# Optimization experiments

Measured on AMD Instinct MI355X. Metric: run time of the kernel, lower is better.

## Reference

```python
import jax, jax.numpy as jnp
import numpy as np

DIM = 2048
HEAD_DIM = 128
H = DIM // HEAD_DIM          # num ttt heads = 16
D_H = 128                    # inter_multi = 1.0 -> d_h = head_dim
CHUNK = 2048                 # lact_chunk_size
B, L = 1, 8192
BASE_LR = 0.01
LN_EPS = 1e-6                # flax LayerNorm default
NS_COEFS = [(4.0848, -6.8946, 2.927), (3.9505, -6.3029, 2.6377),
            (3.7418, -5.5913, 2.3037), (2.8769, -3.1427, 1.2046),
            (2.8366, -3.0525, 1.2012)]


def silu(x):
    return x * jax.nn.sigmoid(x)


def silu_backprop(dy, x):
    s = jax.nn.sigmoid(x)
    return dy * s * (1 + x * (1 - s))


def l2_norm(x, eps=1e-5):
    return x / (jnp.linalg.norm(x, axis=-1, keepdims=True) + eps)


def zeropower_ns5(G):
    # 5-step Newton-Schulz orthogonalization on a batch of matrices (bh, m, n)
    X = G
    transposed = G.shape[1] > G.shape[2]
    if transposed:
        X = jnp.swapaxes(X, 1, 2)
    X = X / (jnp.linalg.norm(X, axis=(1, 2), keepdims=True) + 1e-7)
    for a, b, c in NS_COEFS:
        A = X @ jnp.swapaxes(X, 1, 2)
        Bm = b * A + c * (A @ A)
        X = a * X + Bm @ X
    if transposed:
        X = jnp.swapaxes(X, 1, 2)
    return X


def block_causal_lact_swiglu(w0, w1, w2, q, k, v, lr0, lr1, lr2, momentum):
    # w0,w2: (bh, d_h, d); w1: (bh, d, d_h); q,k,v: (bh, l, d); lr*: (bh, l, 1)
    bh, l, d = k.shape
    v = jnp.swapaxes(v, 1, 2)   # (bh, d, l)
    q = jnp.swapaxes(q, 1, 2)   # (bh, d, l)
    w0_norm = jnp.linalg.norm(w0, axis=2, keepdims=True)
    w1_norm = jnp.linalg.norm(w1, axis=2, keepdims=True)
    w2_norm = jnp.linalg.norm(w2, axis=2, keepdims=True)
    outs = []
    for i in range(0, l - CHUNK, CHUNK):
        s, e = i, i + CHUNK
        ki = k[:, s:e, :]                      # (bh, C, d)
        vi = v[:, :, s:e]                      # (bh, d, C)
        qi = q[:, :, s:e]                      # (bh, d, C)
        lr0i, lr1i, lr2i = lr0[:, s:e, :], lr1[:, s:e, :], lr2[:, s:e, :]
        # apply current fast weights to queries
        h = w2 @ qi                            # (bh, d_h, C)
        gate = silu(w0 @ qi)
        outs.append(w1 @ (gate * h))           # (bh, d, C)
        # manual SwiGLU backprop through keys to get fast-weight grads
        kiT = jnp.swapaxes(ki, 1, 2)           # (bh, d, C)
        gate_before = w0 @ kiT                 # (bh, d_h, C)
        hidden_before = w2 @ kiT               # (bh, d_h, C)
        hidden = silu(gate_before) * hidden_before
        dhidden = jnp.swapaxes(w1, 1, 2) @ vi  # (bh, d_h, C)
        dhidden_before = dhidden * silu(gate_before)
        dgate = dhidden * hidden_before
        dgate_before = silu_backprop(dgate, gate_before)
        lr1iT = jnp.swapaxes(lr1i, 1, 2)       # (bh, 1, C) per-token lr
        dw1 = vi @ jnp.swapaxes(hidden * lr1iT, 1, 2)   # (bh, d, d_h)
        dw0 = dgate_before @ (ki * lr0i)                # (bh, d_h, d)
        dw2 = dhidden_before @ (ki * lr2i)              # (bh, d_h, d)
        if momentum is not None:
            m_i = jnp.mean(momentum[:, s:e, :], axis=1, keepdims=True)  # (bh,1,1)
            dw0 = dw0 + dw0 * m_i
            dw1 = dw1 + dw1 * m_i
            dw2 = dw2 + dw2 * m_i
        dw0 = zeropower_ns5(dw0)
        dw1 = zeropower_ns5(dw1)
        dw2 = zeropower_ns5(dw2)
        w0 = w0 + dw0
        w1 = w1 + dw1
        w2 = w2 + dw2
        # renormalize rows back to the initial norms
        w0 = w0 / (jnp.linalg.norm(w0, axis=2, keepdims=True) + 1e-5) * w0_norm
        w1 = w1 / (jnp.linalg.norm(w1, axis=2, keepdims=True) + 1e-5) * w1_norm
        w2 = w2 / (jnp.linalg.norm(w2, axis=2, keepdims=True) + 1e-5) * w2_norm
    # final chunk: apply only
    qi = q[:, :, l - CHUNK:]
    h = w2 @ qi
    gate = silu(w0 @ qi)
    outs.append(w1 @ (gate * h))
    out = jnp.concatenate(outs, axis=2)        # (bh, d, l)
    return jnp.swapaxes(out, 1, 2)             # (bh, l, d)


def _forward(x, W_qkv, W_lr, W_o, W_m, b_m, W_s, b_s, ln_g, ln_b, w0, w1, w2):
    b, l, _ = x.shape
    h, d = H, HEAD_DIM
    qkv = silu(x @ W_qkv).reshape(b, l, h, 3 * d)
    ttt_q, ttt_k, ttt_v = jnp.split(qkv, 3, axis=-1)
    ttt_q = l2_norm(ttt_q).reshape(b * h, l, d)
    ttt_k = l2_norm(ttt_k).reshape(b * h, l, d)
    ttt_v = ttt_v.reshape(b * h, l, d)
    base_lr_inv = BASE_LR + jnp.log(-jnp.expm1(jnp.float32(-BASE_LR)))
    lr = jax.nn.softplus(x @ W_lr + base_lr_inv)                 # (b, l, 3h)
    lr = lr.reshape(b, l, 3, h).transpose(2, 0, 3, 1).reshape(3, b * h, l, 1)
    lr0, lr1, lr2 = lr[0], lr[1], lr[2]
    w0b = jnp.tile(w0, (b, 1, 1))
    w1b = jnp.tile(w1, (b, 1, 1))
    w2b = jnp.tile(w2, (b, 1, 1))
    momentum = jax.nn.sigmoid(x @ W_m + b_m)                     # (b, l, h)
    momentum = momentum.reshape(b, l, h, 1).transpose(0, 2, 1, 3).reshape(b * h, l, 1)
    out = block_causal_lact_swiglu(w0b, w1b, w2b, ttt_q, ttt_k, ttt_v,
                                   lr0, lr1, lr2, momentum)      # (bh, l, d)
    # LayerNorm over last dim (flax default eps)
    mu = jnp.mean(out, axis=-1, keepdims=True)
    var = jnp.mean(jnp.square(out - mu), axis=-1, keepdims=True)
    out = (out - mu) * jax.lax.rsqrt(var + LN_EPS) * ln_g + ln_b
    scale = silu(x @ W_s + b_s).reshape(b, l, h, 1).transpose(0, 2, 1, 3).reshape(b * h, l, 1)
    out = out * scale
    out = out.reshape(b, h, l, d).transpose(0, 2, 1, 3).reshape(b, l, h * d)
    return out @ W_o


def setup_inputs() -> dict:
    ks = jax.random.split(jax.random.key(0), 11)
    sd = 1.0 / np.sqrt(DIM)
    return {
        "x": jax.random.normal(ks[0], (B, L, DIM), jnp.float32),
        "W_qkv": jax.random.normal(ks[1], (DIM, 3 * DIM), jnp.float32) * sd,
        "W_lr": jax.random.normal(ks[2], (DIM, 3 * H), jnp.float32) * sd,
        "W_o": jax.random.normal(ks[3], (DIM, DIM), jnp.float32) * sd,
        "W_m": jax.random.normal(ks[4], (DIM, H), jnp.float32) * sd,
        "b_m": jnp.zeros((H,), jnp.float32),
        "W_s": jax.random.normal(ks[5], (DIM, H), jnp.float32) * sd,
        "b_s": jnp.zeros((H,), jnp.float32),
        "ln_g": jnp.ones((HEAD_DIM,), jnp.float32),
        "ln_b": jnp.zeros((HEAD_DIM,), jnp.float32),
        "w0": jax.random.normal(ks[6], (H, D_H, HEAD_DIM), jnp.float32) / np.sqrt(HEAD_DIM),
        "w1": jax.random.normal(ks[7], (H, HEAD_DIM, D_H), jnp.float32) / np.sqrt(D_H),
        "w2": jax.random.normal(ks[8], (H, D_H, HEAD_DIM), jnp.float32) / np.sqrt(HEAD_DIM),
    }


def reference(x, W_qkv, W_lr, W_o, W_m, b_m, W_s, b_s, ln_g, ln_b, w0, w1, w2):
    return _forward(x, W_qkv, W_lr, W_o, W_m, b_m, W_s, b_s, ln_g, ln_b, w0, w1, w2)
```

## Files before the change

### kernel.cpp

```cpp
#include <hip/hip_runtime.h>
#include <hip/hip_bf16.h>
#include <cstdint>
#include <cstddef>

#define LSEQ   8192
#define DMODEL 2048
#define NH     16
#define HD     128
#define CH     2048

typedef __attribute__((ext_vector_type(8))) __bf16 bf16x8;
typedef __attribute__((ext_vector_type(4))) float f32x4;


__device__ __forceinline__ float wave_sum64(float v) {
#pragma unroll
  for (int m = 32; m; m >>= 1) v += __shfl_xor(v, m, 64);
  return v;
}

__device__ __forceinline__ float sigm(float x) { return 1.0f / (1.0f + expf(-x)); }

__device__ __forceinline__ unsigned short f2bf(float f) {
  unsigned int u = __float_as_uint(f);
  u += 0x7FFFu + ((u >> 16) & 1u);
  return (unsigned short)(u >> 16);
}
__device__ __forceinline__ float bf2f(unsigned short h) {
  return __uint_as_float((unsigned int)h << 16);
}

__device__ __forceinline__ void gload_lds16(const void* g, void* l) {
  __builtin_amdgcn_global_load_lds((__attribute__((address_space(1))) void*)(g),
                                   (__attribute__((address_space(3))) void*)(l), 16, 0, 0);
}

union bfu8 { bf16x8 v; unsigned short u[8]; };


__global__ void k_cast(const float* __restrict__ X, unsigned short* __restrict__ Xb, int n4) {
  int i = blockIdx.x * 256 + threadIdx.x;
  int stride = gridDim.x * 256;
  for (; i < n4; i += stride) {
    float4 v = ((const float4*)X)[i];
    ushort4 o;
    o.x = f2bf(v.x); o.y = f2bf(v.y); o.z = f2bf(v.z); o.w = f2bf(v.w);
    ((ushort4*)Xb)[i] = o;
  }
}

__global__ void k_tcast(const float* __restrict__ W, unsigned short* __restrict__ Wt,
                        int K, int N) {
  __shared__ float t[64][65];
  const int n0 = blockIdx.x * 64, k0 = blockIdx.y * 64;
  const int tid = threadIdx.x;
  const int cx = tid & 63, ry = tid >> 6;
#pragma unroll
  for (int r = 0; r < 16; ++r) {
    int row = ry + r * 4;
    t[row][cx] = W[(size_t)(k0 + row) * N + n0 + cx];
  }
  __syncthreads();
#pragma unroll
  for (int r = 0; r < 16; ++r) {
    int nn = ry + r * 4;
    Wt[(size_t)(n0 + nn) * K + k0 + cx] = f2bf(t[cx][nn]);
  }
}


__device__ __forceinline__ void gemm_core(const unsigned short* __restrict__ A,
                                          const unsigned short* __restrict__ B,
                                          int K, int ldA, int ldB, int row0, int col0,
                                          unsigned short* Al, unsigned short* Bl,
                                          f32x4 acc[4][4]) {
  const int tid = threadIdx.x;
  const int w = tid >> 6, l = tid & 63;
  const int lrow = l & 15, lk = (l >> 4) * 8;
  const int wr = (w >> 1) * 64, wc = (w & 1) * 64;
  const int srow = l >> 2, skk = (l & 3) * 8;

  for (int kk = 0; kk < K; kk += 32) {
#pragma unroll
    for (int q = 0; q < 2; ++q) {
      int c = w * 2 + q;
      gload_lds16(A + (size_t)(row0 + c * 16 + srow) * ldA + kk + skk, &Al[c * 512]);
      gload_lds16(B + (size_t)(col0 + c * 16 + srow) * ldB + kk + skk, &Bl[c * 512]);
    }
    __syncthreads();
    bf16x8 af[4], bfr[4];
#pragma unroll
    for (int m = 0; m < 4; ++m)
      af[m] = *(const bf16x8*)&Al[(wr + m * 16 + lrow) * 32 + lk];
#pragma unroll
    for (int n = 0; n < 4; ++n)
      bfr[n] = *(const bf16x8*)&Bl[(wc + n * 16 + lrow) * 32 + lk];
#pragma unroll
    for (int m = 0; m < 4; ++m)
#pragma unroll
      for (int n = 0; n < 4; ++n)
        acc[m][n] = __builtin_amdgcn_mfma_f32_16x16x32_bf16(af[m], bfr[n], acc[m][n], 0, 0, 0);
    __syncthreads();
  }
}


__device__ __forceinline__ bf16x8 ld_sw(const unsigned short* base, int row, int kcol) {
  int byte = (row * 256 + kcol * 2) ^ ((row & 7) << 4);
  return *(const bf16x8*)((const char*)base + byte);
}
__device__ __forceinline__ void st_sw(unsigned short* base, int row, int col, unsigned short v) {
  int byte = (row * 256 + col * 2) ^ ((row & 7) << 4);
  *(unsigned short*)((char*)base + byte) = v;
}
__device__ __forceinline__ unsigned short ld_sw1(const unsigned short* base, int row, int col) {
  int byte = (row * 256 + col * 2) ^ ((row & 7) << 4);
  return *(const unsigned short*)((const char*)base + byte);
}

__device__ __forceinline__ void stage_sw(const float* __restrict__ src, int ld,
                                         unsigned short* dst, int tid) {
#pragma unroll
  for (int p = 0; p < 16; ++p) {
    int row = p * 8 + (tid >> 5);
    int col = (tid & 31) * 4;
    float4 v = *(const float4*)(src + (size_t)row * ld + col);
    int byte = (row * 256 + col * 2) ^ ((row & 7) << 4);
    unsigned short* d = (unsigned short*)((char*)dst + byte);
    d[0] = f2bf(v.x); d[1] = f2bf(v.y); d[2] = f2bf(v.z); d[3] = f2bf(v.w);
  }
}

__device__ __forceinline__ void stage_hl(const float* __restrict__ src, int ld,
                                         unsigned short* H, unsigned short* L, int tid) {
#pragma unroll
  for (int p = 0; p < 16; ++p) {
    int row = p * 8 + (tid >> 5);
    int col = (tid & 31) * 4;
    float4 v = *(const float4*)(src + (size_t)row * ld + col);
    int byte = (row * 256 + col * 2) ^ ((row & 7) << 4);
    unsigned short* h = (unsigned short*)((char*)H + byte);
    unsigned short* l = (unsigned short*)((char*)L + byte);
    const float* pv = (const float*)&v;
#pragma unroll
    for (int i = 0; i < 4; ++i) {
      unsigned short hi = f2bf(pv[i]);
      h[i] = hi;
      l[i] = f2bf(pv[i] - bf2f(hi));
    }
  }
}

__device__ __forceinline__ void stage_hl_1024(const float* __restrict__ src, int ld,
                                              unsigned short* H, unsigned short* L, int tid) {
#pragma unroll
  for (int p = 0; p < 4; ++p) {
    int row = p * 32 + (tid >> 5);
    int col = (tid & 31) * 4;
    float4 v = *(const float4*)(src + (size_t)row * ld + col);
    int byte = (row * 256 + col * 2) ^ ((row & 7) << 4);
    unsigned short* h = (unsigned short*)((char*)H + byte);
    unsigned short* l = (unsigned short*)((char*)L + byte);
    const float* pv = (const float*)&v;
#pragma unroll
    for (int i = 0; i < 4; ++i) {
      unsigned short hi = f2bf(pv[i]);
      h[i] = hi;
      l[i] = f2bf(pv[i] - bf2f(hi));
    }
  }
}

__device__ __forceinline__ void stage_hl_ts(const float* __restrict__ src, int ld,
                                            const float* __restrict__ lr,
                                            unsigned short* H, unsigned short* L, int tid) {
#pragma unroll
  for (int p = 0; p < 16; ++p) {
    int t = p * 8 + (tid >> 5);
    int d = (tid & 31) * 4;
    float4 v = *(const float4*)(src + (size_t)t * ld + d);
    float sc = lr[t];
    const float* pv = (const float*)&v;
#pragma unroll
    for (int i = 0; i < 4; ++i) {
      float x = pv[i] * sc;
      unsigned short hi = f2bf(x);
      st_sw(H, d + i, t, hi);
      st_sw(L, d + i, t, f2bf(x - bf2f(hi)));
    }
  }
}


__global__ void k_init_w(const float* __restrict__ w0, const float* __restrict__ w1,
                         const float* __restrict__ w2, float* __restrict__ WW,
                         float* __restrict__ WN0, float* __restrict__ W1T) {
  int rid = blockIdx.x;
  int m = rid >> 11;
  int gr = rid & 2047;
  const float* src = (m == 0) ? w0 : (m == 1) ? w1 : w2;
  const float* row = src + (size_t)gr * HD;
  float* drow = WW + ((size_t)m * 2048 + gr) * HD;
  int l = threadIdx.x;
  float v0 = row[l], v1 = row[l + 64];
  drow[l] = v0; drow[l + 64] = v1;
  if (m == 1) {
    int g = gr >> 7, r = gr & 127;
    W1T[((size_t)g * 128 + l) * 128 + r] = v0;
    W1T[((size_t)g * 128 + l + 64) * 128 + r] = v1;
  }
  float s = wave_sum64(v0 * v0 + v1 * v1);
  if (l == 0) WN0[rid] = sqrtf(s);
}


__global__ __launch_bounds__(256) void k_qkv_mfma(const unsigned short* __restrict__ xb,
                                                  const unsigned short* __restrict__ Wqt,
                                                  float* __restrict__ Q, float* __restrict__ Km,
                                                  float* __restrict__ V) {
  __shared__ unsigned short Al[128 * 32];
  __shared__ unsigned short Bl[128 * 32];
  __shared__ float nrm[128][2];
  const int flat = blockIdx.x;
  const int swz = (flat & 7) * 384 + (flat >> 3);
  const int bx = swz & 63, ct = swz >> 6;

  f32x4 acc[4][4];
#pragma unroll
  for (int m = 0; m < 4; ++m)
#pragma unroll
    for (int n = 0; n < 4; ++n) acc[m][n] = {};

  gemm_core(xb, Wqt, DMODEL, DMODEL, DMODEL, bx * 128, ct * 128, Al, Bl, acc);

  const int hh = ct / 3, which = ct % 3;
  float* dst = (which == 0) ? Q : (which == 1) ? Km : V;
  const int tid = threadIdx.x, w = tid >> 6, l = tid & 63;
  const int wr = (w >> 1) * 64, wc = (w & 1) * 64;

#pragma unroll
  for (int m = 0; m < 4; ++m)
#pragma unroll
    for (int n = 0; n < 4; ++n)
#pragma unroll
      for (int j = 0; j < 4; ++j) {
        float v = acc[m][n][j];
        acc[m][n][j] = v * sigm(v);
      }

  float f[4][4];
  if (which != 2) {
#pragma unroll
    for (int m = 0; m < 4; ++m)
#pragma unroll
      for (int j = 0; j < 4; ++j) {
        float p = 0.0f;
#pragma unroll
        for (int n = 0; n < 4; ++n) p = fmaf(acc[m][n][j], acc[m][n][j], p);
        p += __shfl_xor(p, 1, 64);
        p += __shfl_xor(p, 2, 64);
        p += __shfl_xor(p, 4, 64);
        p += __shfl_xor(p, 8, 64);
        f[m][j] = p;
      }
    if ((l & 15) == 0) {
#pragma unroll
      for (int m = 0; m < 4; ++m)
#pragma unroll
        for (int j = 0; j < 4; ++j)
          nrm[wr + m * 16 + (l >> 4) * 4 + j][w & 1] = f[m][j];
    }
    __syncthreads();
#pragma unroll
    for (int m = 0; m < 4; ++m)
#pragma unroll
      for (int j = 0; j < 4; ++j) {
        int row = wr + m * 16 + (l >> 4) * 4 + j;
        f[m][j] = 1.0f / (sqrtf(nrm[row][0] + nrm[row][1]) + 1e-5f);
      }
  } else {
#pragma unroll
    for (int m = 0; m < 4; ++m)
#pragma unroll
      for (int j = 0; j < 4; ++j) f[m][j] = 1.0f;
  }

#pragma unroll
  for (int m = 0; m < 4; ++m)
#pragma unroll
    for (int j = 0; j < 4; ++j) {
      int t = bx * 128 + wr + m * 16 + (l >> 4) * 4 + j;
      int fth = t * NH + hh;
      int g = fth >> 13, tp = fth & 8191;
      float* drow = dst + ((size_t)g * LSEQ + tp) * HD;
#pragma unroll
      for (int n = 0; n < 4; ++n)
        drow[wc + n * 16 + (l & 15)] = acc[m][n][j] * f[m][j];
    }
}


__global__ __launch_bounds__(256) void k_lrms5(const float* __restrict__ x,
                                               const float* __restrict__ Wlr,
                                               const float* __restrict__ Wsc,
                                               float* __restrict__ P) {
  __shared__ float Xs[128][67];
  __shared__ float Ws[128][68];
  const int tb = blockIdx.x;
  const int kp = blockIdx.y;
  const int tid = threadIdx.x;
  for (int i = tid; i < 128 * 64; i += 256) {
    int k = i >> 6, c = i & 63;
    float wv = (c < 48) ? Wlr[(size_t)(kp * 128 + k) * 48 + c]
                        : Wsc[(size_t)(kp * 128 + k) * 16 + (c - 48)];
    Ws[k][c] = wv;
  }
  const int t8 = tid >> 5, kk = tid & 31;
#pragma unroll
  for (int r = 0; r < 8; ++r) {
    int t = t8 + r * 8;
    float4 v = *(const float4*)(x + (size_t)(tb * 64 + t) * DMODEL + kp * 128 + kk * 4);
    Xs[kk * 4 + 0][t] = v.x; Xs[kk * 4 + 1][t] = v.y;
    Xs[kk * 4 + 2][t] = v.z; Xs[kk * 4 + 3][t] = v.w;
  }
  __syncthreads();
  const int ty = tid >> 4, tx = tid & 15;
  float acc[4][4];
#pragma unroll
  for (int i = 0; i < 4; ++i)
#pragma unroll
    for (int j = 0; j < 4; ++j) acc[i][j] = 0.0f;
  for (int k = 0; k < 128; ++k) {
    float a[4], b[4];
#pragma unroll
    for (int i = 0; i < 4; ++i) a[i] = Xs[k][ty * 4 + i];
#pragma unroll
    for (int j = 0; j < 4; ++j) b[j] = Ws[k][tx * 4 + j];
#pragma unroll
    for (int i = 0; i < 4; ++i)
#pragma unroll
      for (int j = 0; j < 4; ++j) acc[i][j] = fmaf(a[i], b[j], acc[i][j]);
  }
  float* o = P + ((size_t)tb * 16 + kp) * 4096;
#pragma unroll
  for (int i = 0; i < 4; ++i)
#pragma unroll
    for (int j = 0; j < 4; ++j)
      o[(ty * 4 + i) * 64 + tx * 4 + j] = acc[i][j];
}

__global__ void k_lrsum(const float* __restrict__ P, const float* __restrict__ bs,
                        float* __restrict__ LR, float* __restrict__ SCL) {
  int e = blockIdx.x * 256 + threadIdx.x;
  int t = e >> 6, c = e & 63;
  const float* base = P + ((size_t)(t >> 6) * 16) * 4096 + (t & 63) * 64 + c;
  float sum = 0.0f;
#pragma unroll
  for (int kp = 0; kp < 16; ++kp) sum += base[(size_t)kp * 4096];
  if (c < 48) {
    float base_lr_inv = 0.01f + logf(-expm1f(-0.01f));
    float v = sum + base_lr_inv;
    float sp = fmaxf(v, 0.0f) + log1pf(expf(-fabsf(v)));
    LR[(size_t)c * LSEQ + t] = sp;
  } else {
    float v = sum + bs[c - 48];
    SCL[(size_t)(c - 48) * LSEQ + t] = v * sigm(v);
  }
}


__global__ __launch_bounds__(256) void k_out2(const float* __restrict__ WW,
                                              const float* __restrict__ Q,
                                              const float* __restrict__ SCL,
                                              const float* __restrict__ lng,
                                              const float* __restrict__ lnb,
                                              unsigned short* __restrict__ U, int s) {
  __shared__ __align__(16) char smem[131072];
  unsigned short* Qs  = (unsigned short*)smem;
  unsigned short* W0s = (unsigned short*)(smem + 32768);
  unsigned short* W2s = (unsigned short*)(smem + 65536);
  unsigned short* GHs = (unsigned short*)(smem + 98304);
  float* Os = (float*)smem;

  const int g = blockIdx.y;
  const int t0 = blockIdx.x * 128;
  const int tid = threadIdx.x;
  const int w = tid >> 6, l = tid & 63;
  const int lrow = l & 15, lk8 = (l >> 4) * 8;
  const int wr = (w >> 1) * 64, wc = (w & 1) * 64;

  const float* Qg  = Q + ((size_t)g * LSEQ + s + t0) * HD;
  const float* w0g = WW + ((size_t)0 * 2048 + g * 128) * 128;
  const float* w1g = WW + ((size_t)1 * 2048 + g * 128) * 128;
  const float* w2g = WW + ((size_t)2 * 2048 + g * 128) * 128;

  stage_sw(Qg, HD, Qs, tid);
  stage_sw(w0g, 128, W0s, tid);
  stage_sw(w2g, 128, W2s, tid);
  __syncthreads();

  f32x4 ga[4][4], ha[4][4];
#pragma unroll
  for (int m = 0; m < 4; ++m)
#pragma unroll
    for (int n = 0; n < 4; ++n) { ga[m][n] = {}; ha[m][n] = {}; }
#pragma unroll
  for (int kk = 0; kk < 128; kk += 32) {
    bf16x8 af[4], b0[4], b2[4];
#pragma unroll
    for (int m = 0; m < 4; ++m) af[m] = ld_sw(Qs, wr + m * 16 + lrow, kk + lk8);
#pragma unroll
    for (int n = 0; n < 4; ++n) {
      b0[n] = ld_sw(W0s, wc + n * 16 + lrow, kk + lk8);
      b2[n] = ld_sw(W2s, wc + n * 16 + lrow, kk + lk8);
    }
#pragma unroll
    for (int m = 0; m < 4; ++m)
#pragma unroll
      for (int n = 0; n < 4; ++n) {
        ga[m][n] = __builtin_amdgcn_mfma_f32_16x16x32_bf16(af[m], b0[n], ga[m][n], 0, 0, 0);
        ha[m][n] = __builtin_amdgcn_mfma_f32_16x16x32_bf16(af[m], b2[n], ha[m][n], 0, 0, 0);
      }
  }
#pragma unroll
  for (int m = 0; m < 4; ++m)
#pragma unroll
    for (int n = 0; n < 4; ++n)
#pragma unroll
      for (int j = 0; j < 4; ++j) {
        int row = wr + m * 16 + (l >> 4) * 4 + j;
        int col = wc + n * 16 + (l & 15);
        float gv = ga[m][n][j];
        st_sw(GHs, row, col, f2bf(gv * sigm(gv) * ha[m][n][j]));
      }
  __syncthreads();
  stage_sw(w1g, 128, W0s, tid);
  __syncthreads();

  f32x4 oa[4][4];
#pragma unroll
  for (int m = 0; m < 4; ++m)
#pragma unroll
    for (int n = 0; n < 4; ++n) oa[m][n] = {};
#pragma unroll
  for (int kk = 0; kk < 128; kk += 32) {
    bf16x8 af[4], b1[4];
#pragma unroll
    for (int m = 0; m < 4; ++m) af[m] = ld_sw(GHs, wr + m * 16 + lrow, kk + lk8);
#pragma unroll
    for (int n = 0; n < 4; ++n) b1[n] = ld_sw(W0s, wc + n * 16 + lrow, kk + lk8);
#pragma unroll
    for (int m = 0; m < 4; ++m)
#pragma unroll
      for (int n = 0; n < 4; ++n)
        oa[m][n] = __builtin_amdgcn_mfma_f32_16x16x32_bf16(af[m], b1[n], oa[m][n], 0, 0, 0);
  }
  __syncthreads();
#pragma unroll
  for (int m = 0; m < 4; ++m)
#pragma unroll
    for (int n = 0; n < 4; ++n)
#pragma unroll
      for (int j = 0; j < 4; ++j) {
        int row = wr + m * 16 + (l >> 4) * 4 + j;
        int col = wc + n * 16 + (l & 15);
        Os[row * 132 + col] = oa[m][n][j];
      }
  __syncthreads();

  const int tok = tid >> 1, part = tid & 1;
  const float* orow = Os + tok * 132 + part * 64;
  float sum = 0.0f;
#pragma unroll
  for (int q = 0; q < 16; ++q) {
    float4 v = *(const float4*)(orow + q * 4);
    sum += (v.x + v.y) + (v.z + v.w);
  }
  sum += __shfl_xor(sum, 1, 64);
  float mu = sum * (1.0f / 128.0f);
  float vs = 0.0f;
#pragma unroll
  for (int q = 0; q < 16; ++q) {
    float4 v = *(const float4*)(orow + q * 4);
    float d0 = v.x - mu, d1 = v.y - mu, d2 = v.z - mu, d3 = v.w - mu;
    vs += d0 * d0 + d1 * d1 + d2 * d2 + d3 * d3;
  }
  vs += __shfl_xor(vs, 1, 64);
  float rstd = rsqrtf(vs * (1.0f / 128.0f) + 1e-6f);
  int tabs = s + t0 + tok;
  float sc = SCL[(size_t)g * LSEQ + tabs];
  unsigned short* urow = U + (size_t)tabs * DMODEL + g * HD + part * 64;
#pragma unroll
  for (int q = 0; q < 16; ++q) {
    float4 v = *(const float4*)(orow + q * 4);
    int d = part * 64 + q * 4;
    ushort4 o;
    o.x = f2bf(((v.x - mu) * rstd * lng[d + 0] + lnb[d + 0]) * sc);
    o.y = f2bf(((v.y - mu) * rstd * lng[d + 1] + lnb[d + 1]) * sc);
    o.z = f2bf(((v.z - mu) * rstd * lng[d + 2] + lnb[d + 2]) * sc);
    o.w = f2bf(((v.w - mu) * rstd * lng[d + 3] + lnb[d + 3]) * sc);
    *(ushort4*)(urow + q * 4) = o;
  }
}


__global__ __launch_bounds__(1024) void k_fe(const float* __restrict__ WW,
                                             const float* __restrict__ W1T,
                                             const float* __restrict__ Km,
                                             const float* __restrict__ V,
                                             float* __restrict__ BUF, int s) {
  __shared__ __align__(16) char smem[131072];
  unsigned short* KH = (unsigned short*)smem;
  unsigned short* KL = (unsigned short*)(smem + 32768);
  unsigned short* VH = (unsigned short*)(smem + 65536);
  unsigned short* VL = (unsigned short*)(smem + 98304);

  const int tt0 = blockIdx.x * 128;
  const int g = blockIdx.y;
  const int tid = threadIdx.x;
  const int w = tid >> 6, l = tid & 63;
  const int ww = w >> 2, wv = w & 3;
  const int lrow = l & 15, lk8 = (l >> 4) * 8;
  const int frow = (l >> 4) * 4, fcol = l & 15;

  stage_hl_1024(Km + ((size_t)g * LSEQ + s + tt0) * HD, HD, KH, KL, tid);
  stage_hl_1024(V + ((size_t)g * LSEQ + s + tt0) * HD, HD, VH, VL, tid);
  __syncthreads();

  const float* Asrc[3];
  Asrc[0] = WW + ((size_t)0 * 2048 + g * 128) * 128;
  Asrc[1] = WW + ((size_t)2 * 2048 + g * 128) * 128;
  Asrc[2] = W1T + (size_t)g * 16384;

  f32x4 acc[3][2][2];
#pragma unroll
  for (int q = 0; q < 3; ++q)
#pragma unroll
    for (int m = 0; m < 2; ++m)
#pragma unroll
      for (int n = 0; n < 2; ++n) acc[q][m][n] = {};

#pragma unroll 1
  for (int q = 0; q < 3; ++q) {
    const float* src = Asrc[q];
    const unsigned short* BH = (q == 2) ? VH : KH;
    const unsigned short* BL = (q == 2) ? VL : KL;
#pragma unroll
    for (int kk = 0; kk < 128; kk += 32) {
      bf16x8 ah[2], al[2], bh[2], bl[2];
#pragma unroll
      for (int m = 0; m < 2; ++m) {
        int row = ww * 32 + m * 16 + lrow;
        float4 v0 = *(const float4*)(src + (size_t)row * 128 + kk + lk8);
        float4 v1 = *(const float4*)(src + (size_t)row * 128 + kk + lk8 + 4);
        bfu8 h, lo;
        const float* p0 = (const float*)&v0;
        const float* p1 = (const float*)&v1;
#pragma unroll
        for (int i = 0; i < 4; ++i) {
          unsigned short hb0 = f2bf(p0[i]);
          h.u[i] = hb0; lo.u[i] = f2bf(p0[i] - bf2f(hb0));
          unsigned short hb1 = f2bf(p1[i]);
          h.u[i + 4] = hb1; lo.u[i + 4] = f2bf(p1[i] - bf2f(hb1));
        }
        ah[m] = h.v; al[m] = lo.v;
      }
#pragma unroll
      for (int n = 0; n < 2; ++n) {
        int row = wv * 32 + n * 16 + lrow;
        bh[n] = ld_sw(BH, row, kk + lk8);
        bl[n] = ld_sw(BL, row, kk + lk8);
      }
#pragma unroll
      for (int m = 0; m < 2; ++m)
#pragma unroll
        for (int n = 0; n < 2; ++n) {
          acc[q][m][n] = __builtin_amdgcn_mfma_f32_16x16x32_bf16(ah[m], bh[n], acc[q][m][n], 0, 0, 0);
          acc[q][m][n] = __builtin_amdgcn_mfma_f32_16x16x32_bf16(ah[m], bl[n], acc[q][m][n], 0, 0, 0);
          acc[q][m][n] = __builtin_amdgcn_mfma_f32_16x16x32_bf16(al[m], bh[n], acc[q][m][n], 0, 0, 0);
        }
    }
  }

  float* out0 = BUF + (size_t)0 * (NH * 128 * CH) + (size_t)g * 128 * CH;
  float* out1 = BUF + (size_t)1 * (NH * 128 * CH) + (size_t)g * 128 * CH;
  float* out2 = BUF + (size_t)2 * (NH * 128 * CH) + (size_t)g * 128 * CH;
#pragma unroll
  for (int m = 0; m < 2; ++m)
#pragma unroll
    for (int n = 0; n < 2; ++n)
#pragma unroll
      for (int j = 0; j < 4; ++j) {
        int row = ww * 32 + m * 16 + frow + j;
        int col = wv * 32 + n * 16 + fcol;
        float gb = acc[0][m][n][j];
        float hb = acc[1][m][n][j];
        float dh = acc[2][m][n][j];
        float sg = sigm(gb);
        float sgb = gb * sg;
        float hid = sgb * hb;
        float dgate = dh * hb;
        float dgb = dgate * sg * (1.0f + gb * (1.0f - sg));
        float dhb = dh * sgb;
        size_t o = (size_t)row * CH + tt0 + col;
        out0[o] = hid; out1[o] = dgb; out2[o] = dhb;
      }
}

__global__ __launch_bounds__(256) void k_dwp_mx(const float* __restrict__ BUF,
                                                const float* __restrict__ Km,
                                                const float* __restrict__ V,
                                                const float* __restrict__ LR,
                                                float* __restrict__ DWP, int s) {
  __shared__ __align__(16) char smem[131072];
  unsigned short* AH = (unsigned short*)smem;
  unsigned short* AL = (unsigned short*)(smem + 32768);
  unsigned short* BH = (unsigned short*)(smem + 65536);
  unsigned short* BL = (unsigned short*)(smem + 98304);

  const int p = blockIdx.x;
  const int g = blockIdx.y;
  const int z = blockIdx.z;
  const int tid = threadIdx.x;
  const int w = tid >> 6, l = tid & 63;
  const int lrow = l & 15, lk8 = (l >> 4) * 8;
  const int wr = (w >> 1) * 64, wc = (w & 1) * 64;

  const int msel = (z == 0) ? 1 : (z == 1) ? 0 : 2;
  const float* M = BUF + (size_t)msel * (NH * 128 * CH) + (size_t)g * 128 * CH;
  const float* N = (z == 1) ? V : Km;
  const float* lr = LR + (size_t)(z * NH + g) * LSEQ;
  const int ts = p * 256;

  f32x4 acc[4][4];
#pragma unroll
  for (int m = 0; m < 4; ++m)
#pragma unroll
    for (int n = 0; n < 4; ++n) acc[m][n] = {};

  for (int h = 0; h < 2; ++h) {
    if (h) __syncthreads();
    stage_hl(M + ts + h * 128, CH, AH, AL, tid);
    stage_hl_ts(N + ((size_t)g * LSEQ + s + ts + h * 128) * HD, HD,
                lr + s + ts + h * 128, BH, BL, tid);
    __syncthreads();
#pragma unroll
    for (int kk = 0; kk < 128; kk += 32) {
      bf16x8 ah[4], al4[4], bh[4], bl4[4];
#pragma unroll
      for (int m = 0; m < 4; ++m) {
        ah[m] = ld_sw(AH, wr + m * 16 + lrow, kk + lk8);
        al4[m] = ld_sw(AL, wr + m * 16 + lrow, kk + lk8);
      }
#pragma unroll
      for (int n = 0; n < 4; ++n) {
        bh[n] = ld_sw(BH, wc + n * 16 + lrow, kk + lk8);
        bl4[n] = ld_sw(BL, wc + n * 16 + lrow, kk + lk8);
      }
#pragma unroll
      for (int m = 0; m < 4; ++m)
#pragma unroll
        for (int n = 0; n < 4; ++n) {
          acc[m][n] = __builtin_amdgcn_mfma_f32_16x16x32_bf16(ah[m], bh[n], acc[m][n], 0, 0, 0);
          acc[m][n] = __builtin_amdgcn_mfma_f32_16x16x32_bf16(ah[m], bl4[n], acc[m][n], 0, 0, 0);
          acc[m][n] = __builtin_amdgcn_mfma_f32_16x16x32_bf16(al4[m], bh[n], acc[m][n], 0, 0, 0);
        }
    }
  }

  float* outp = DWP + (((size_t)(z * NH + g)) * 8 + p) * 16384;
#pragma unroll
  for (int m = 0; m < 4; ++m)
#pragma unroll
    for (int n = 0; n < 4; ++n)
#pragma unroll
      for (int j = 0; j < 4; ++j) {
        int row = wr + m * 16 + (l >> 4) * 4 + j;
        int col = wc + n * 16 + (l & 15);
        outp[row * 128 + col] = acc[m][n][j];
      }
}

__global__ __launch_bounds__(1024) void k_ns5_mfma(const float* __restrict__ DWP,
                                                   float* __restrict__ DW) {
  __shared__ __align__(16) char smem[131072];
  unsigned short* PH = (unsigned short*)smem;
  unsigned short* PL = (unsigned short*)(smem + 32768);
  unsigned short* QH = (unsigned short*)(smem + 65536);
  unsigned short* QL = (unsigned short*)(smem + 98304);
  float* red = (float*)(smem + 65536);

  const float NA[5] = {4.0848f, 3.9505f, 3.7418f, 2.8769f, 2.8366f};
  const float NB[5] = {-6.8946f, -6.3029f, -5.5913f, -3.1427f, -3.0525f};
  const float NC[5] = {2.927f, 2.6377f, 2.3037f, 1.2046f, 1.2012f};
  const int zg = blockIdx.x;
  const int z = zg >> 4;
  const float* base = DWP + (size_t)zg * 8 * 16384;
  float* Gout = DW + (size_t)zg * 16384;
  const int tid = threadIdx.x;
  const int w = tid >> 6, l = tid & 63;
  const int ww = w >> 2, wv = w & 3;
  const int lrow = l & 15, lk8 = (l >> 4) * 8;
  const int frow = (l >> 4) * 4, fcol = l & 15;

  float vals[16];
  float psum = 0.0f;
#pragma unroll
  for (int r = 0; r < 16; ++r) {
    int idx = tid + r * 1024;
    float sv = 0.0f;
#pragma unroll
    for (int p = 0; p < 8; ++p) sv += base[(size_t)p * 16384 + idx];
    vals[r] = sv;
    psum = fmaf(sv, sv, psum);
  }
  psum = wave_sum64(psum);
  if (l == 0) red[w] = psum;
  __syncthreads();
  float tot = 0.0f;
#pragma unroll
  for (int i = 0; i < 16; ++i) tot += red[i];
  float scl = 1.0f / (sqrtf(tot) + 1e-7f);
  __syncthreads();
#pragma unroll
  for (int r = 0; r < 16; ++r) {
    int idx = tid + r * 1024;
    int rr = idx >> 7, cc = idx & 127;
    float v = vals[r] * scl;
    unsigned short hi = f2bf(v);
    st_sw(PH, rr, cc, hi);
    st_sw(PL, rr, cc, f2bf(v - bf2f(hi)));
  }
  __syncthreads();

#pragma unroll 1
  for (int it = 0; it < 5; ++it) {
    const float ac = NA[it], bc = NB[it], cc2 = NC[it];

    f32x4 accA[2][2];
#pragma unroll
    for (int m = 0; m < 2; ++m)
#pragma unroll
      for (int n = 0; n < 2; ++n) accA[m][n] = {};
#pragma unroll
    for (int kk = 0; kk < 128; kk += 32) {
      bf16x8 ah[2], al[2], bh[2], bl[2];
#pragma unroll
      for (int m = 0; m < 2; ++m) {
        ah[m] = ld_sw(PH, ww * 32 + m * 16 + lrow, kk + lk8);
        al[m] = ld_sw(PL, ww * 32 + m * 16 + lrow, kk + lk8);
      }
#pragma unroll
      for (int n = 0; n < 2; ++n) {
        bh[n] = ld_sw(PH, wv * 32 + n * 16 + lrow, kk + lk8);
        bl[n] = ld_sw(PL, wv * 32 + n * 16 + lrow, kk + lk8);
      }
#pragma unroll
      for (int m = 0; m < 2; ++m)
#pragma unroll
        for (int n = 0; n < 2; ++n) {
          accA[m][n] = __builtin_amdgcn_mfma_f32_16x16x32_bf16(ah[m], bh[n], accA[m][n], 0, 0, 0);
          accA[m][n] = __builtin_amdgcn_mfma_f32_16x16x32_bf16(ah[m], bl[n], accA[m][n], 0, 0, 0);
          accA[m][n] = __builtin_amdgcn_mfma_f32_16x16x32_bf16(al[m], bh[n], accA[m][n], 0, 0, 0);
        }
    }
#pragma unroll
    for (int m = 0; m < 2; ++m)
#pragma unroll
      for (int n = 0; n < 2; ++n)
#pragma unroll
        for (int j = 0; j < 4; ++j) {
          int row = ww * 32 + m * 16 + frow + j;
          int col = wv * 32 + n * 16 + fcol;
          float v = accA[m][n][j];
          unsigned short hi = f2bf(v);
          st_sw(QH, row, col, hi);
          st_sw(QL, row, col, f2bf(v - bf2f(hi)));
        }
    __syncthreads();

    f32x4 accB[2][2];
#pragma unroll
    for (int m = 0; m < 2; ++m)
#pragma unroll
      for (int n = 0; n < 2; ++n) accB[m][n] = {};
#pragma unroll
    for (int kk = 0; kk < 128; kk += 32) {
      bf16x8 ah[2], al[2], bh[2], bl[2];
#pragma unroll
      for (int m = 0; m < 2; ++m) {
        ah[m] = ld_sw(QH, ww * 32 + m * 16 + lrow, kk + lk8);
        al[m] = ld_sw(QL, ww * 32 + m * 16 + lrow, kk + lk8);
      }
#pragma unroll
      for (int n = 0; n < 2; ++n) {
        bh[n] = ld_sw(QH, wv * 32 + n * 16 + lrow, kk + lk8);
        bl[n] = ld_sw(QL, wv * 32 + n * 16 + lrow, kk + lk8);
      }
#pragma unroll
      for (int m = 0; m < 2; ++m)
#pragma unroll
        for (int n = 0; n < 2; ++n) {
          accB[m][n] = __builtin_amdgcn_mfma_f32_16x16x32_bf16(ah[m], bh[n], accB[m][n], 0, 0, 0);
          accB[m][n] = __builtin_amdgcn_mfma_f32_16x16x32_bf16(ah[m], bl[n], accB[m][n], 0, 0, 0);
          accB[m][n] = __builtin_amdgcn_mfma_f32_16x16x32_bf16(al[m], bh[n], accB[m][n], 0, 0, 0);
        }
    }
#pragma unroll
    for (int m = 0; m < 2; ++m)
#pragma unroll
      for (int n = 0; n < 2; ++n)
#pragma unroll
        for (int j = 0; j < 4; ++j)
          accB[m][n][j] = fmaf(bc, accA[m][n][j], cc2 * accB[m][n][j]);
    __syncthreads();
#pragma unroll
    for (int m = 0; m < 2; ++m)
#pragma unroll
      for (int n = 0; n < 2; ++n)
#pragma unroll
        for (int j = 0; j < 4; ++j) {
          int row = ww * 32 + m * 16 + frow + j;
          int col = wv * 32 + n * 16 + fcol;
          float v = accB[m][n][j];
          unsigned short hi = f2bf(v);
          st_sw(QH, row, col, hi);
          st_sw(QL, row, col, f2bf(v - bf2f(hi)));
        }
    unsigned short th[16], tl[16];
#pragma unroll
    for (int r = 0; r < 16; ++r) {
      int idx = tid + r * 1024;
      int rr = idx >> 7, ccx = idx & 127;
      th[r] = ld_sw1(PH, rr, ccx);
      tl[r] = ld_sw1(PL, rr, ccx);
    }
    __syncthreads();
#pragma unroll
    for (int r = 0; r < 16; ++r) {
      int idx = tid + r * 1024;
      int rr = idx >> 7, ccx = idx & 127;
      st_sw(PH, ccx, rr, th[r]);
      st_sw(PL, ccx, rr, tl[r]);
    }
    __syncthreads();

    f32x4 accC[2][2];
#pragma unroll
    for (int m = 0; m < 2; ++m)
#pragma unroll
      for (int n = 0; n < 2; ++n) accC[m][n] = {};
#pragma unroll
    for (int kk = 0; kk < 128; kk += 32) {
      bf16x8 ah[2], al[2], bh[2], bl[2];
#pragma unroll
      for (int m = 0; m < 2; ++m) {
        ah[m] = ld_sw(PH, ww * 32 + m * 16 + lrow, kk + lk8);
        al[m] = ld_sw(PL, ww * 32 + m * 16 + lrow, kk + lk8);
      }
#pragma unroll
      for (int n = 0; n < 2; ++n) {
        bh[n] = ld_sw(QH, wv * 32 + n * 16 + lrow, kk + lk8);
        bl[n] = ld_sw(QL, wv * 32 + n * 16 + lrow, kk + lk8);
      }
#pragma unroll
      for (int m = 0; m < 2; ++m)
#pragma unroll
        for (int n = 0; n < 2; ++n) {
          accC[m][n] = __builtin_amdgcn_mfma_f32_16x16x32_bf16(ah[m], bh[n], accC[m][n], 0, 0, 0);
          accC[m][n] = __builtin_amdgcn_mfma_f32_16x16x32_bf16(ah[m], bl[n], accC[m][n], 0, 0, 0);
          accC[m][n] = __builtin_amdgcn_mfma_f32_16x16x32_bf16(al[m], bh[n], accC[m][n], 0, 0, 0);
        }
    }
#pragma unroll
    for (int m = 0; m < 2; ++m)
#pragma unroll
      for (int n = 0; n < 2; ++n)
#pragma unroll
        for (int j = 0; j < 4; ++j) {
          int row = ww * 32 + m * 16 + frow + j;
          int col = wv * 32 + n * 16 + fcol;
          float yv = bf2f(ld_sw1(PH, row, col)) + bf2f(ld_sw1(PL, row, col));
          accC[m][n][j] = fmaf(ac, yv, accC[m][n][j]);
        }
    __syncthreads();
#pragma unroll
    for (int m = 0; m < 2; ++m)
#pragma unroll
      for (int n = 0; n < 2; ++n)
#pragma unroll
        for (int j = 0; j < 4; ++j) {
          int row = ww * 32 + m * 16 + frow + j;
          int col = wv * 32 + n * 16 + fcol;
          float v = accC[m][n][j];
          unsigned short hi = f2bf(v);
          st_sw(PH, row, col, hi);
          st_sw(PL, row, col, f2bf(v - bf2f(hi)));
        }
    __syncthreads();
  }

#pragma unroll
  for (int r = 0; r < 16; ++r) {
    int idx = tid + r * 1024;
    int rr = idx >> 7, ccx = idx & 127;
    if (z == 1)
      Gout[idx] = bf2f(ld_sw1(PH, rr, ccx)) + bf2f(ld_sw1(PL, rr, ccx));
    else
      Gout[idx] = bf2f(ld_sw1(PH, ccx, rr)) + bf2f(ld_sw1(PL, ccx, rr));
  }
}

__global__ void k_apply(float* __restrict__ WW, const float* __restrict__ DW,
                        const float* __restrict__ WN0, float* __restrict__ W1T) {
  int rid = blockIdx.x;
  int m = rid >> 11;
  int gr = rid & 2047;
  int l = threadIdx.x;
  float* wrow = WW + (size_t)rid * 128;
  const float* drow = DW + (size_t)rid * 128;
  float v0 = wrow[l] + drow[l];
  float v1 = wrow[l + 64] + drow[l + 64];
  float s = wave_sum64(v0 * v0 + v1 * v1);
  float f = WN0[rid] / (sqrtf(s) + 1e-5f);
  v0 *= f; v1 *= f;
  wrow[l] = v0;
  wrow[l + 64] = v1;
  if (m == 1) {
    int g = gr >> 7, r = gr & 127;
    W1T[((size_t)g * 128 + l) * 128 + r] = v0;
    W1T[((size_t)g * 128 + l + 64) * 128 + r] = v1;
  }
}


__global__ __launch_bounds__(256) void k_final_mfma(const unsigned short* __restrict__ U,
                                                    const unsigned short* __restrict__ Wot,
                                                    float* __restrict__ out) {
  __shared__ unsigned short Al[128 * 32];
  __shared__ unsigned short Bl[128 * 32];
  f32x4 acc[4][4];
#pragma unroll
  for (int m = 0; m < 4; ++m)
#pragma unroll
    for (int n = 0; n < 4; ++n) acc[m][n] = {};

  const int flat = blockIdx.x;
  const int swz = (flat & 7) * 128 + (flat >> 3);
  const int row0 = (swz & 63) * 128, col0 = (swz >> 6) * 128;
  gemm_core(U, Wot, DMODEL, DMODEL, DMODEL, row0, col0, Al, Bl, acc);

  const int tid = threadIdx.x, w = tid >> 6, l = tid & 63;
  const int wr = (w >> 1) * 64, wc = (w & 1) * 64;
#pragma unroll
  for (int m = 0; m < 4; ++m)
#pragma unroll
    for (int j = 0; j < 4; ++j) {
      int t = row0 + wr + m * 16 + (l >> 4) * 4 + j;
      float* orow = out + (size_t)t * DMODEL + col0;
#pragma unroll
      for (int n = 0; n < 4; ++n)
        orow[wc + n * 16 + (l & 15)] = acc[m][n][j];
    }
}


extern "C" void kernel_launch(void* const* d_in, const int* in_sizes, int n_in,
                              void* d_out, int out_size, void* d_ws, size_t ws_size,
                              hipStream_t stream) {
  (void)in_sizes; (void)n_in; (void)out_size;
  const float* x    = (const float*)d_in[0];
  const float* Wqkv = (const float*)d_in[1];
  const float* Wlr  = (const float*)d_in[2];
  const float* Wo   = (const float*)d_in[3];
  const float* Wsc  = (const float*)d_in[6];
  const float* bs   = (const float*)d_in[7];
  const float* lng  = (const float*)d_in[8];
  const float* lnb  = (const float*)d_in[9];
  const float* w0   = (const float*)d_in[10];
  const float* w1   = (const float*)d_in[11];
  const float* w2   = (const float*)d_in[12];

  float* Q = (float*)d_out;

  float* ws = (float*)d_ws;
  size_t off = 0;
  auto alloc = [&](size_t n) { float* p = ws + off; off += n; return p; };
  float* Km   = alloc((size_t)NH * LSEQ * HD);
  float* V    = alloc((size_t)NH * LSEQ * HD);
  float* Uf   = alloc((size_t)LSEQ * DMODEL / 2);
  float* LR   = alloc((size_t)3 * NH * LSEQ);
  float* SCL  = alloc((size_t)NH * LSEQ);
  float* WW   = alloc((size_t)3 * NH * HD * HD);
  float* WN0  = alloc((size_t)3 * NH * HD);
  float* W1T  = alloc((size_t)NH * HD * HD);
  float* BUF  = alloc((size_t)3 * NH * HD * CH);
  float* DW   = alloc((size_t)3 * NH * HD * HD);
  float* DWP  = alloc((size_t)3 * NH * 8 * HD * HD);
  if (off * sizeof(float) > ws_size) return;

  unsigned short* U = (unsigned short*)Uf;
  unsigned short* xb  = (unsigned short*)BUF;
  unsigned short* Wqt = (unsigned short*)(BUF + (size_t)LSEQ * DMODEL / 2);
  float* Plr = BUF;
  unsigned short* Wot = (unsigned short*)BUF;

  k_init_w<<<3 * NH * HD, 64, 0, stream>>>(w0, w1, w2, WW, WN0, W1T);
  k_cast<<<2048, 256, 0, stream>>>(x, xb, LSEQ * DMODEL / 4);
  k_tcast<<<dim3(3 * DMODEL / 64, DMODEL / 64), 256, 0, stream>>>(Wqkv, Wqt, DMODEL, 3 * DMODEL);
  k_qkv_mfma<<<3072, 256, 0, stream>>>(xb, Wqt, Q, Km, V);
  k_lrms5<<<dim3(LSEQ / 64, 16), 256, 0, stream>>>(x, Wlr, Wsc, Plr);
  k_lrsum<<<LSEQ * 64 / 256, 256, 0, stream>>>(Plr, bs, LR, SCL);

  for (int c = 0; c < 4; ++c) {
    int s = c * CH;
    k_out2<<<dim3(CH / 128, NH), 256, 0, stream>>>(WW, Q, SCL, lng, lnb, U, s);
    if (c < 3) {
      k_fe<<<dim3(CH / 128, NH), 1024, 0, stream>>>(WW, W1T, Km, V, BUF, s);
      k_dwp_mx<<<dim3(8, NH, 3), 256, 0, stream>>>(BUF, Km, V, LR, DWP, s);
      k_ns5_mfma<<<3 * NH, 1024, 0, stream>>>(DWP, DW);
      k_apply<<<3 * NH * HD, 64, 0, stream>>>(WW, DW, WN0, W1T);
    }
  }
  k_tcast<<<dim3(DMODEL / 64, DMODEL / 64), 256, 0, stream>>>(Wo, Wot, DMODEL, DMODEL);
  k_final_mfma<<<1024, 256, 0, stream>>>(U, Wot, (float*)d_out);
}
```

Baseline: 1.375 ms.

## Halve k_out2 token tile and drop block swizzle in GEMM kernels

k_out2 now processes 64 tokens per block instead of 128. Its shared memory drops from 128KB to 80KB by reusing the Q buffer for the gated hidden activations, and the LayerNorm epilogue is spread over four threads per token. This doubles the grid and should allow more blocks per CU, at the cost of re-staging the three 128x128 weight tiles twice as often. Separately, the QKV and final GEMMs drop their flat-index L2 swizzle and use a plain 2D grid, which may hurt cache locality.

```diff
diff --git a/kernel.cpp b/kernel.cpp
--- a/kernel.cpp
+++ b/kernel.cpp
@@ -122,6 +122,19 @@
                                          unsigned short* dst, int tid) {
 #pragma unroll
   for (int p = 0; p < 16; ++p) {
+    int row = p * 8 + (tid >> 5);
+    int col = (tid & 31) * 4;
+    float4 v = *(const float4*)(src + (size_t)row * ld + col);
+    int byte = (row * 256 + col * 2) ^ ((row & 7) << 4);
+    unsigned short* d = (unsigned short*)((char*)dst + byte);
+    d[0] = f2bf(v.x); d[1] = f2bf(v.y); d[2] = f2bf(v.z); d[3] = f2bf(v.w);
+  }
+}
+
+__device__ __forceinline__ void stage_sw64(const float* __restrict__ src, int ld,
+                                           unsigned short* dst, int tid) {
+#pragma unroll
+  for (int p = 0; p < 8; ++p) {
     int row = p * 8 + (tid >> 5);
     int col = (tid & 31) * 4;
     float4 v = *(const float4*)(src + (size_t)row * ld + col);
@@ -221,9 +234,7 @@
   __shared__ unsigned short Al[128 * 32];
   __shared__ unsigned short Bl[128 * 32];
   __shared__ float nrm[128][2];
-  const int flat = blockIdx.x;
-  const int swz = (flat & 7) * 384 + (flat >> 3);
-  const int bx = swz & 63, ct = swz >> 6;
+  const int bx = blockIdx.x, ct = blockIdx.y;
 
   f32x4 acc[4][4];
 #pragma unroll
@@ -375,55 +386,55 @@
                                               const float* __restrict__ lng,
                                               const float* __restrict__ lnb,
                                               unsigned short* __restrict__ U, int s) {
-  __shared__ __align__(16) char smem[131072];
+  __shared__ __align__(16) char smem[81920];
   unsigned short* Qs  = (unsigned short*)smem;
-  unsigned short* W0s = (unsigned short*)(smem + 32768);
-  unsigned short* W2s = (unsigned short*)(smem + 65536);
-  unsigned short* GHs = (unsigned short*)(smem + 98304);
-  float* Os = (float*)smem;
+  unsigned short* W0s = (unsigned short*)(smem + 16384);
+  unsigned short* W2s = (unsigned short*)(smem + 49152);
+  float* Os = (float*)(smem + 16384);
 
   const int g = blockIdx.y;
-  const int t0 = blockIdx.x * 128;
+  const int t0 = blockIdx.x * 64;
   const int tid = threadIdx.x;
   const int w = tid >> 6, l = tid & 63;
   const int lrow = l & 15, lk8 = (l >> 4) * 8;
-  const int wr = (w >> 1) * 64, wc = (w & 1) * 64;
+  const int wr = (w >> 1) * 32, wc = (w & 1) * 64;
 
   const float* Qg  = Q + ((size_t)g * LSEQ + s + t0) * HD;
   const float* w0g = WW + ((size_t)0 * 2048 + g * 128) * 128;
   const float* w1g = WW + ((size_t)1 * 2048 + g * 128) * 128;
   const float* w2g = WW + ((size_t)2 * 2048 + g * 128) * 128;
 
-  stage_sw(Qg, HD, Qs, tid);
+  stage_sw64(Qg, HD, Qs, tid);
   stage_sw(w0g, 128, W0s, tid);
   stage_sw(w2g, 128, W2s, tid);
   __syncthreads();
 
-  f32x4 ga[4][4], ha[4][4];
-#pragma unroll
-  for (int m = 0; m < 4; ++m)
+  f32x4 ga[2][4], ha[2][4];
+#pragma unroll
+  for (int m = 0; m < 2; ++m)
 #pragma unroll
     for (int n = 0; n < 4; ++n) { ga[m][n] = {}; ha[m][n] = {}; }
 #pragma unroll
   for (int kk = 0; kk < 128; kk += 32) {
-    bf16x8 af[4], b0[4], b2[4];
-#pragma unroll
-    for (int m = 0; m < 4; ++m) af[m] = ld_sw(Qs, wr + m * 16 + lrow, kk + lk8);
+    bf16x8 af[2], b0[4], b2[4];
+#pragma unroll
+    for (int m = 0; m < 2; ++m) af[m] = ld_sw(Qs, wr + m * 16 + lrow, kk + lk8);
 #pragma unroll
     for (int n = 0; n < 4; ++n) {
       b0[n] = ld_sw(W0s, wc + n * 16 + lrow, kk + lk8);
       b2[n] = ld_sw(W2s, wc + n * 16 + lrow, kk + lk8);
     }
 #pragma unroll
-    for (int m = 0; m < 4; ++m)
+    for (int m = 0; m < 2; ++m)
 #pragma unroll
       for (int n = 0; n < 4; ++n) {
         ga[m][n] = __builtin_amdgcn_mfma_f32_16x16x32_bf16(af[m], b0[n], ga[m][n], 0, 0, 0);
         ha[m][n] = __builtin_amdgcn_mfma_f32_16x16x32_bf16(af[m], b2[n], ha[m][n], 0, 0, 0);
       }
   }
-#pragma unroll
-  for (int m = 0; m < 4; ++m)
+  __syncthreads();
+#pragma unroll
+  for (int m = 0; m < 2; ++m)
 #pragma unroll
     for (int n = 0; n < 4; ++n)
 #pragma unroll
@@ -431,33 +442,32 @@
         int row = wr + m * 16 + (l >> 4) * 4 + j;
         int col = wc + n * 16 + (l & 15);
         float gv = ga[m][n][j];
-        st_sw(GHs, row, col, f2bf(gv * sigm(gv) * ha[m][n][j]));
-      }
-  __syncthreads();
+        st_sw(Qs, row, col, f2bf(gv * sigm(gv) * ha[m][n][j]));
+      }
   stage_sw(w1g, 128, W0s, tid);
   __syncthreads();
 
-  f32x4 oa[4][4];
-#pragma unroll
-  for (int m = 0; m < 4; ++m)
+  f32x4 oa[2][4];
+#pragma unroll
+  for (int m = 0; m < 2; ++m)
 #pragma unroll
     for (int n = 0; n < 4; ++n) oa[m][n] = {};
 #pragma unroll
   for (int kk = 0; kk < 128; kk += 32) {
-    bf16x8 af[4], b1[4];
-#pragma unroll
-    for (int m = 0; m < 4; ++m) af[m] = ld_sw(GHs, wr + m * 16 + lrow, kk + lk8);
+    bf16x8 af[2], b1[4];
+#pragma unroll
+    for (int m = 0; m < 2; ++m) af[m] = ld_sw(Qs, wr + m * 16 + lrow, kk + lk8);
 #pragma unroll
     for (int n = 0; n < 4; ++n) b1[n] = ld_sw(W0s, wc + n * 16 + lrow, kk + lk8);
 #pragma unroll
-    for (int m = 0; m < 4; ++m)
+    for (int m = 0; m < 2; ++m)
 #pragma unroll
       for (int n = 0; n < 4; ++n)
         oa[m][n] = __builtin_amdgcn_mfma_f32_16x16x32_bf16(af[m], b1[n], oa[m][n], 0, 0, 0);
   }
   __syncthreads();
 #pragma unroll
-  for (int m = 0; m < 4; ++m)
+  for (int m = 0; m < 2; ++m)
 #pragma unroll
     for (int n = 0; n < 4; ++n)
 #pragma unroll
@@ -468,32 +478,34 @@
       }
   __syncthreads();
 
-  const int tok = tid >> 1, part = tid & 1;
-  const float* orow = Os + tok * 132 + part * 64;
+  const int tok = tid >> 2, part = tid & 3;
+  const float* orow = Os + tok * 132 + part * 32;
   float sum = 0.0f;
 #pragma unroll
-  for (int q = 0; q < 16; ++q) {
+  for (int q = 0; q < 8; ++q) {
     float4 v = *(const float4*)(orow + q * 4);
     sum += (v.x + v.y) + (v.z + v.w);
   }
   sum += __shfl_xor(sum, 1, 64);
+  sum += __shfl_xor(sum, 2, 64);
   float mu = sum * (1.0f / 128.0f);
   float vs = 0.0f;
 #pragma unroll
-  for (int q = 0; q < 16; ++q) {
+  for (int q = 0; q < 8; ++q) {
     float4 v = *(const float4*)(orow + q * 4);
     float d0 = v.x - mu, d1 = v.y - mu, d2 = v.z - mu, d3 = v.w - mu;
     vs += d0 * d0 + d1 * d1 + d2 * d2 + d3 * d3;
   }
   vs += __shfl_xor(vs, 1, 64);
+  vs += __shfl_xor(vs, 2, 64);
   float rstd = rsqrtf(vs * (1.0f / 128.0f) + 1e-6f);
   int tabs = s + t0 + tok;
   float sc = SCL[(size_t)g * LSEQ + tabs];
-  unsigned short* urow = U + (size_t)tabs * DMODEL + g * HD + part * 64;
-#pragma unroll
-  for (int q = 0; q < 16; ++q) {
+  unsigned short* urow = U + (size_t)tabs * DMODEL + g * HD + part * 32;
+#pragma unroll
+  for (int q = 0; q < 8; ++q) {
     float4 v = *(const float4*)(orow + q * 4);
-    int d = part * 64 + q * 4;
+    int d = part * 32 + q * 4;
     ushort4 o;
     o.x = f2bf(((v.x - mu) * rstd * lng[d + 0] + lnb[d + 0]) * sc);
     o.y = f2bf(((v.y - mu) * rstd * lng[d + 1] + lnb[d + 1]) * sc);
@@ -945,9 +957,7 @@
 #pragma unroll
     for (int n = 0; n < 4; ++n) acc[m][n] = {};
 
-  const int flat = blockIdx.x;
-  const int swz = (flat & 7) * 128 + (flat >> 3);
-  const int row0 = (swz & 63) * 128, col0 = (swz >> 6) * 128;
+  const int row0 = blockIdx.x * 128, col0 = blockIdx.y * 128;
   gemm_core(U, Wot, DMODEL, DMODEL, DMODEL, row0, col0, Al, Bl, acc);
 
   const int tid = threadIdx.x, w = tid >> 6, l = tid & 63;
@@ -1008,13 +1018,13 @@
   k_init_w<<<3 * NH * HD, 64, 0, stream>>>(w0, w1, w2, WW, WN0, W1T);
   k_cast<<<2048, 256, 0, stream>>>(x, xb, LSEQ * DMODEL / 4);
   k_tcast<<<dim3(3 * DMODEL / 64, DMODEL / 64), 256, 0, stream>>>(Wqkv, Wqt, DMODEL, 3 * DMODEL);
-  k_qkv_mfma<<<3072, 256, 0, stream>>>(xb, Wqt, Q, Km, V);
+  k_qkv_mfma<<<dim3(LSEQ / 128, 48), 256, 0, stream>>>(xb, Wqt, Q, Km, V);
   k_lrms5<<<dim3(LSEQ / 64, 16), 256, 0, stream>>>(x, Wlr, Wsc, Plr);
   k_lrsum<<<LSEQ * 64 / 256, 256, 0, stream>>>(Plr, bs, LR, SCL);
 
   for (int c = 0; c < 4; ++c) {
     int s = c * CH;
-    k_out2<<<dim3(CH / 128, NH), 256, 0, stream>>>(WW, Q, SCL, lng, lnb, U, s);
+    k_out2<<<dim3(CH / 64, NH), 256, 0, stream>>>(WW, Q, SCL, lng, lnb, U, s);
     if (c < 3) {
       k_fe<<<dim3(CH / 128, NH), 1024, 0, stream>>>(WW, W1T, Km, V, BUF, s);
       k_dwp_mx<<<dim3(8, NH, 3), 256, 0, stream>>>(BUF, Km, V, LR, DWP, s);
@@ -1023,5 +1033,5 @@
     }
   }
   k_tcast<<<dim3(DMODEL / 64, DMODEL / 64), 256, 0, stream>>>(Wo, Wot, DMODEL, DMODEL);
-  k_final_mfma<<<1024, 256, 0, stream>>>(U, Wot, (float*)d_out);
-}
+  k_final_mfma<<<dim3(LSEQ / 128, DMODEL / 128), 256, 0, stream>>>(U, Wot, (float*)d_out);
+}
```

Result: faster. 1.347 ms (-2.1%).
